# Performance work log

Hardware: AMD Instinct MI355X
Metric: run time of the kernel (lower is better)

## Reference

```python
import jax, jax.numpy as jnp
import numpy as np

EMBED_DIM = 512
NUM_HEADS = 8
HEAD_DIM = EMBED_DIM // NUM_HEADS


def setup_inputs() -> dict:
    key = jax.random.key(0)
    ks = jax.random.split(key, 6)
    B, S, D = 2, 4096, EMBED_DIM
    scale = 1.0 / np.sqrt(D)
    inputs = jax.random.normal(ks[0], (B, S, D), dtype=jnp.float32)
    Wq = jax.random.normal(ks[1], (D, D), dtype=jnp.float32) * scale
    Wk = jax.random.normal(ks[2], (D, D), dtype=jnp.float32) * scale
    Wv = jax.random.normal(ks[3], (D, D), dtype=jnp.float32) * scale
    Wo = jax.random.normal(ks[4], (D, D), dtype=jnp.float32) * scale
    zeros = jnp.zeros((D,), dtype=jnp.float32)
    return {"inputs": inputs, "Wq": Wq, "bq": zeros, "Wk": Wk, "bk": zeros,
            "Wv": Wv, "bv": zeros, "Wo": Wo, "bo": zeros}


def _split_heads(x, B, S):
    # [B,S,D] -> [B,H,S,hd]
    return x.reshape(B, S, NUM_HEADS, HEAD_DIM).transpose(0, 2, 1, 3)


def reference(inputs, Wq, bq, Wk, bk, Wv, bv, Wo, bo):
    B, S, D = inputs.shape
    q = _split_heads(inputs @ Wq + bq, B, S)
    k = _split_heads(inputs @ Wk + bk, B, S)
    v = _split_heads(inputs @ Wv + bv, B, S)
    scale = 1.0 / jnp.sqrt(jnp.asarray(HEAD_DIM, dtype=inputs.dtype))
    # full [B,H,S,S] score matrix, as in the original naive SDPA
    scores = jnp.einsum('bhqd,bhkd->bhqk', q, k) * scale
    weights = jax.nn.softmax(scores, axis=-1)
    attn = jnp.einsum('bhqk,bhkd->bhqd', weights, v)
    attn = attn.transpose(0, 2, 1, 3).reshape(B, S, D)
    return attn @ Wo + bo
```

## Files before the change

kernel.cpp:

```cpp
#include <hip/hip_runtime.h>
#include <hip/hip_bf16.h>
#include <stdint.h>


typedef __bf16 bf16x8 __attribute__((ext_vector_type(8)));
typedef float f32x4 __attribute__((ext_vector_type(4)));
typedef float f32x16 __attribute__((ext_vector_type(16)));

using as1_void = __attribute__((address_space(1))) void;
using as3_void = __attribute__((address_space(3))) void;

__device__ __forceinline__ void gload16(const void* g, void* l) {
    __builtin_amdgcn_global_load_lds((const as1_void*)g, (as3_void*)l, 16, 0, 0);
}

__device__ __forceinline__ f32x4 mfma16(bf16x8 a, bf16x8 b, f32x4 c) {
    return __builtin_amdgcn_mfma_f32_16x16x32_bf16(a, b, c, 0, 0, 0);
}

__device__ __forceinline__ f32x16 mfma32(bf16x8 a, bf16x8 b, f32x16 c) {
    return __builtin_amdgcn_mfma_f32_32x32x16_bf16(a, b, c, 0, 0, 0);
}

__device__ __forceinline__ uint32_t pkbf(float a, float b) {
    union { __hip_bfloat16 h[2]; uint32_t u; } r;
    r.h[0] = __float2bfloat16(a);
    r.h[1] = __float2bfloat16(b);
    return r.u;
}

__device__ __forceinline__ void pl32swap(uint32_t& a, uint32_t& b) {
#if __has_builtin(__builtin_amdgcn_permlane32_swap)
    typedef unsigned int uint32x2_t __attribute__((ext_vector_type(2)));
    uint32x2_t r = __builtin_amdgcn_permlane32_swap(a, b, false, false);
    a = r[0];
    b = r[1];
#else
    asm volatile("v_permlane32_swap_b32 %0, %1" : "+v"(a), "+v"(b));
#endif
}

__global__ void cvt_all(const float* __restrict__ X, __hip_bfloat16* __restrict__ Xb,
                        const float* __restrict__ w0, const float* __restrict__ w1,
                        const float* __restrict__ w2, const float* __restrict__ w3,
                        __hip_bfloat16* __restrict__ o0, __hip_bfloat16* __restrict__ o1,
                        __hip_bfloat16* __restrict__ o2, __hip_bfloat16* __restrict__ o3) {
    __shared__ float t[32][33];
    const int bid = blockIdx.x, tid = threadIdx.x;
    if (bid < 1024) {
        const float* W; __hip_bfloat16* O;
        switch (bid >> 8) {
            case 0: W = w0; O = o0; break;
            case 1: W = w1; O = o1; break;
            case 2: W = w2; O = o2; break;
            default: W = w3; O = o3; break;
        }
        int rem = bid & 255;
        int n0 = (rem & 15) * 32, k0 = (rem >> 4) * 32;
        int tx = tid & 31, ty = tid >> 5;
        for (int j = 0; j < 4; ++j)
            t[ty + 8 * j][tx] = W[(size_t)(k0 + ty + 8 * j) * 512 + n0 + tx];
        __syncthreads();
        for (int j = 0; j < 4; ++j)
            O[(size_t)(n0 + ty + 8 * j) * 512 + k0 + tx] = __float2bfloat16(t[tx][ty + 8 * j]);
    } else {
        int i = ((bid - 1024) * 256 + tid) * 4;
        float4 v = *reinterpret_cast<const float4*>(X + i);
        uint2 u;
        u.x = pkbf(v.x, v.y);
        u.y = pkbf(v.z, v.w);
        *reinterpret_cast<uint2*>(Xb + i) = u;
    }
}

__global__ __launch_bounds__(256, 2) void gemm_qkv(
    const __hip_bfloat16* __restrict__ A, const __hip_bfloat16* __restrict__ Bt,
    const float* __restrict__ bq, const float* __restrict__ bk, const float* __restrict__ bv,
    __hip_bfloat16* __restrict__ Qb, __hip_bfloat16* __restrict__ Kb,
    __hip_bfloat16* __restrict__ Vtb, float qs)
{
    const int K = 512;
    __shared__ __hip_bfloat16 Abuf[128 * 32];
    __shared__ __hip_bfloat16 Bbuf[128 * 32];
    const int tid = threadIdx.x, w = tid >> 6, lane = tid & 63;
    const int col = lane & 15, quad = lane >> 4;
    const int wr = w >> 1, wc = w & 1;
    const int tileN = blockIdx.x * 128, tileM = blockIdx.y * 128;

    f32x4 acc[4][4] = {};

    for (int k0 = 0; k0 < K; k0 += 32) {
        for (int i = 0; i < 2; ++i) {
            int g = w * 2 + i;
            int chunk = g * 64 + lane;
            int row = chunk >> 2, c8 = chunk & 3;
            gload16(A + (size_t)(tileM + row) * K + k0 + c8 * 8, Abuf + g * 512);
            gload16(Bt + (size_t)(tileN + row) * K + k0 + c8 * 8, Bbuf + g * 512);
        }
        __syncthreads();
        bf16x8 af[4], bfr[4];
        for (int mt = 0; mt < 4; ++mt)
            af[mt] = *reinterpret_cast<const bf16x8*>(Abuf + (wr * 64 + mt * 16 + col) * 32 + quad * 8);
        for (int nt = 0; nt < 4; ++nt)
            bfr[nt] = *reinterpret_cast<const bf16x8*>(Bbuf + (wc * 64 + nt * 16 + col) * 32 + quad * 8);
        for (int mt = 0; mt < 4; ++mt)
            for (int nt = 0; nt < 4; ++nt)
                acc[mt][nt] = mfma16(af[mt], bfr[nt], acc[mt][nt]);
        __syncthreads();
    }

    const int seg = (tileN + wc * 64) >> 9;
    const float* bias = (seg == 0) ? bq : (seg == 1) ? bk : bv;
    const float scale = (seg == 0) ? qs : 1.0f;
    __hip_bfloat16* outp = (seg == 0) ? Qb : (seg == 1) ? Kb : Vtb;

    for (int mt = 0; mt < 4; ++mt) {
        for (int nt = 0; nt < 4; ++nt) {
            int n = tileN + wc * 64 + nt * 16 + col;
            int nn = n & 511, h = nn >> 6, d = nn & 63;
            float bn = bias[nn];
            for (int r = 0; r < 4; ++r) {
                int m = tileM + wr * 64 + mt * 16 + quad * 4 + r;
                int b = m >> 12, s = m & 4095;
                float v = (acc[mt][nt][r] + bn) * scale;
                size_t off;
                if (seg < 2) off = (((size_t)(b * 8 + h) * 4096 + s) << 6) + d;
                else         off = (((size_t)(b * 8 + h) * 64 + d) << 12) + s;
                outp[off] = __float2bfloat16(v);
            }
        }
    }
}

__global__ __launch_bounds__(256, 2) void gemm_out(
    const __hip_bfloat16* __restrict__ A, const __hip_bfloat16* __restrict__ Bt,
    const float* __restrict__ bias, float* __restrict__ out)
{
    const int N = 512, K = 512;
    __shared__ __hip_bfloat16 Abuf[128 * 32];
    __shared__ __hip_bfloat16 Bbuf[64 * 32];
    const int tid = threadIdx.x, w = tid >> 6, lane = tid & 63;
    const int col = lane & 15, quad = lane >> 4;
    const int tileN = blockIdx.x * 64, tileM = blockIdx.y * 128;

    f32x4 acc[2][4] = {};

    for (int k0 = 0; k0 < K; k0 += 32) {
        for (int i = 0; i < 2; ++i) {
            int g = w * 2 + i;
            int chunk = g * 64 + lane;
            int row = chunk >> 2, c8 = chunk & 3;
            gload16(A + (size_t)(tileM + row) * K + k0 + c8 * 8, Abuf + g * 512);
        }
        {
            int row = tid >> 2, c8 = tid & 3;
            gload16(Bt + (size_t)(tileN + row) * K + k0 + c8 * 8, Bbuf + tid * 8);
        }
        __syncthreads();
        bf16x8 af[2], bfr[4];
        for (int mt = 0; mt < 2; ++mt)
            af[mt] = *reinterpret_cast<const bf16x8*>(Abuf + (w * 32 + mt * 16 + col) * 32 + quad * 8);
        for (int nt = 0; nt < 4; ++nt)
            bfr[nt] = *reinterpret_cast<const bf16x8*>(Bbuf + (nt * 16 + col) * 32 + quad * 8);
        for (int mt = 0; mt < 2; ++mt)
            for (int nt = 0; nt < 4; ++nt)
                acc[mt][nt] = mfma16(af[mt], bfr[nt], acc[mt][nt]);
        __syncthreads();
    }

    for (int mt = 0; mt < 2; ++mt) {
        for (int nt = 0; nt < 4; ++nt) {
            int n = tileN + nt * 16 + col;
            float bn = bias[n];
            for (int r = 0; r < 4; ++r) {
                int m = tileM + w * 32 + mt * 16 + quad * 4 + r;
                out[(size_t)m * N + n] = acc[mt][nt][r] + bn;
            }
        }
    }
}

__global__ __launch_bounds__(256, 2) void flash(
    const __hip_bfloat16* __restrict__ Q,
    const __hip_bfloat16* __restrict__ Kq,
    const __hip_bfloat16* __restrict__ Vt,
    __hip_bfloat16* __restrict__ attnb)
{
    __shared__ __hip_bfloat16 KT[2][4096];
    __shared__ __hip_bfloat16 VB[2][4096];

    const int bh = blockIdx.y, b = bh >> 3, hq = bh & 7;
    const int tid = threadIdx.x, w = tid >> 6, lane = tid & 63;
    const int l31 = lane & 31, hh = lane >> 5, l7 = lane & 7;
    const int q0 = blockIdx.x * 128 + w * 32;

    const __hip_bfloat16* Qh = Q + (size_t)bh * 4096 * 64;
    const __hip_bfloat16* Kh = Kq + (size_t)bh * 4096 * 64;
    const __hip_bfloat16* Vh = Vt + (size_t)bh * 64 * 4096;

    bf16x8 aq[4];
#pragma unroll
    for (int dk = 0; dk < 4; ++dk)
        aq[dk] = *reinterpret_cast<const bf16x8*>(
            Qh + (size_t)(q0 + l31) * 64 + dk * 16 + hh * 8);

    const __hip_bfloat16* ksrc[2];
    const __hip_bfloat16* vsrc[2];
    int ldsoff[2];
#pragma unroll
    for (int i = 0; i < 2; ++i) {
        int c = i * 256 + tid;
        int row = c >> 3, s8 = (c & 7) ^ (row & 7);
        ksrc[i] = Kh + row * 64 + s8 * 8;
        vsrc[i] = Vh + (size_t)row * 4096 + s8 * 8;
        ldsoff[i] = (i * 256 + w * 64) * 8;
    }

    bf16x8 ones;
#pragma unroll
    for (int j = 0; j < 8; ++j) ones[j] = (__bf16)1.0f;

    const f32x16 z16 = {};
    f32x16 o[2] = {};
    f32x16 lacc = {};
    f32x16 sc[2][2];

    gload16(ksrc[0], &KT[0][ldsoff[0]]);
    gload16(ksrc[1], &KT[0][ldsoff[1]]);
    gload16(vsrc[0], &VB[0][ldsoff[0]]);
    gload16(vsrc[1], &VB[0][ldsoff[1]]);
    gload16(ksrc[0] + 4096, &KT[1][ldsoff[0]]);
    gload16(ksrc[1] + 4096, &KT[1][ldsoff[1]]);
    __syncthreads();

#define QK_STEP(KR_, SP2_)                                                      \
    _Pragma("unroll")                                                           \
    for (int kg = 0; kg < 2; ++kg) {                                            \
        _Pragma("unroll")                                                       \
        for (int dk = 0; dk < 4; ++dk) {                                        \
            bf16x8 ak = *reinterpret_cast<const bf16x8*>(                       \
                &KT[KR_][(kg * 32 + l31) * 64 + (((dk * 2 + hh) ^ l7) << 3)]);  \
            sc[SP2_][kg] = (dk == 0) ? mfma32(ak, aq[0], z16)                   \
                                     : mfma32(ak, aq[dk], sc[SP2_][kg]);        \
        }                                                                       \
    }

#define SOFTMAX_EXCHANGE(SP_)                                                   \
    uint32_t U[8][2];                                                           \
    _Pragma("unroll")                                                           \
    for (int kg = 0; kg < 2; ++kg) {                                            \
        f32x16 v = sc[SP_][kg];                                                 \
        _Pragma("unroll")                                                       \
        for (int rr = 0; rr < 4; ++rr) {                                        \
            U[kg * 4 + rr][0] = pkbf(__builtin_amdgcn_exp2f(v[rr * 4 + 0]),     \
                                     __builtin_amdgcn_exp2f(v[rr * 4 + 1]));    \
            U[kg * 4 + rr][1] = pkbf(__builtin_amdgcn_exp2f(v[rr * 4 + 2]),     \
                                     __builtin_amdgcn_exp2f(v[rr * 4 + 3]));    \
        }                                                                       \
    }                                                                           \
    bf16x8 bp[4];                                                               \
    _Pragma("unroll")                                                           \
    for (int kb = 0; kb < 4; ++kb) {                                            \
        _Pragma("unroll")                                                       \
        for (int t2 = 0; t2 < 2; ++t2)                                          \
            pl32swap(U[2 * kb][t2], U[2 * kb + 1][t2]);                         \
        union { uint32_t u[4]; bf16x8 v8; } cc;                                 \
        cc.u[0] = U[2 * kb][0];     cc.u[1] = U[2 * kb][1];                     \
        cc.u[2] = U[2 * kb + 1][0]; cc.u[3] = U[2 * kb + 1][1];                 \
        bp[kb] = cc.v8;                                                         \
    }

#define PV_STEP(VR_)                                                            \
    _Pragma("unroll")                                                           \
    for (int dg = 0; dg < 2; ++dg) {                                            \
        _Pragma("unroll")                                                       \
        for (int kb = 0; kb < 4; ++kb) {                                        \
            bf16x8 av = *reinterpret_cast<const bf16x8*>(                       \
                &VB[VR_][(dg * 32 + l31) * 64 + (((kb * 2 + hh) ^ l7) << 3)]);  \
            o[dg] = mfma32(av, bp[kb], o[dg]);                                  \
        }                                                                       \
    }                                                                           \
    _Pragma("unroll")                                                           \
    for (int kb = 0; kb < 4; ++kb) lacc = mfma32(ones, bp[kb], lacc);

    QK_STEP(0, 0)
    __syncthreads();

#define FLASH_BODY(T_, P_)                                                      \
    {                                                                           \
        const int kt_ = (T_);                                                   \
        int kk = kt_ + 2; if (kk > 63) kk = 63;                                 \
        gload16(ksrc[0] + (size_t)kk * 4096, &KT[(P_)][ldsoff[0]]);             \
        gload16(ksrc[1] + (size_t)kk * 4096, &KT[(P_)][ldsoff[1]]);             \
        gload16(vsrc[0] + (size_t)(kt_ + 1) * 64, &VB[1 - (P_)][ldsoff[0]]);    \
        gload16(vsrc[1] + (size_t)(kt_ + 1) * 64, &VB[1 - (P_)][ldsoff[1]]);    \
        SOFTMAX_EXCHANGE(P_)                                                    \
        QK_STEP(1 - (P_), 1 - (P_))                                             \
        PV_STEP(P_)                                                             \
        __syncthreads();                                                        \
    }

    FLASH_BODY(0, 0)
    for (int kth = 0; kth < 31; ++kth) {
        FLASH_BODY(2 * kth + 1, 1)
        FLASH_BODY(2 * kth + 2, 0)
    }
    {
        SOFTMAX_EXCHANGE(1)
        PV_STEP(1)
    }
#undef FLASH_BODY
#undef PV_STEP
#undef SOFTMAX_EXCHANGE
#undef QK_STEP

    {
        float inv = 1.0f / lacc[0];
        int s = q0 + l31;
        __hip_bfloat16* dst = attnb + ((size_t)b * 4096 + s) * 512 + hq * 64;
#pragma unroll
        for (int dg = 0; dg < 2; ++dg)
#pragma unroll
            for (int rr = 0; rr < 4; ++rr) {
                uint2 u;
                u.x = pkbf(o[dg][rr * 4 + 0] * inv, o[dg][rr * 4 + 1] * inv);
                u.y = pkbf(o[dg][rr * 4 + 2] * inv, o[dg][rr * 4 + 3] * inv);
                *reinterpret_cast<uint2*>(dst + dg * 32 + rr * 8 + hh * 4) = u;
            }
    }
}

extern "C" void kernel_launch(void* const* d_in, const int* in_sizes, int n_in,
                              void* d_out, int out_size, void* d_ws, size_t ws_size,
                              hipStream_t stream) {
    const float* X  = (const float*)d_in[0];
    const float* Wq = (const float*)d_in[1];
    const float* bq = (const float*)d_in[2];
    const float* Wk = (const float*)d_in[3];
    const float* bk = (const float*)d_in[4];
    const float* Wv = (const float*)d_in[5];
    const float* bv = (const float*)d_in[6];
    const float* Wo = (const float*)d_in[7];
    const float* bo = (const float*)d_in[8];
    float* out = (float*)d_out;

    char* ws = (char*)d_ws;
    __hip_bfloat16* Xb  = (__hip_bfloat16*)(ws);
    __hip_bfloat16* Wqt = (__hip_bfloat16*)(ws + ((size_t)8 << 20));
    __hip_bfloat16* Wkt = Wqt + 512 * 512;
    __hip_bfloat16* Wvt = Wkt + 512 * 512;
    __hip_bfloat16* Wot = Wvt + 512 * 512;
    __hip_bfloat16* Qb  = (__hip_bfloat16*)(ws + ((size_t)10 << 20));
    __hip_bfloat16* Kb  = (__hip_bfloat16*)(ws + ((size_t)18 << 20));
    __hip_bfloat16* Vtb = (__hip_bfloat16*)(ws + ((size_t)26 << 20));
    __hip_bfloat16* Atb = (__hip_bfloat16*)(ws + ((size_t)34 << 20));

    cvt_all<<<5120, 256, 0, stream>>>(X, Xb, Wq, Wk, Wv, Wo, Wqt, Wkt, Wvt, Wot);

    const float qs = 0.125f * 1.4426950408889634f;
    gemm_qkv<<<dim3(12, 64), 256, 0, stream>>>(Xb, Wqt, bq, bk, bv, Qb, Kb, Vtb, qs);
    flash<<<dim3(32, 16), 256, 0, stream>>>(Qb, Kb, Vtb, Atb);
    gemm_out<<<dim3(8, 64), 256, 0, stream>>>(Atb, Wot, bo, out);
}
```

Measured before the change: 209.6 us.

## Split attention keys into two halves across blocks and merge partial outputs

The flash kernel grid gains a z dimension of 2, so each block processes only half of the key/value sequence. Each block writes a normalized partial output plus its row sum. A new merge kernel then combines the two partials, weighted by their row sums, before the output projection. This doubles the number of blocks to improve GPU occupancy and latency hiding, at the cost of an extra kernel launch, extra global traffic for the partial outputs, and reuse of workspace and output buffers as scratch.

```diff
diff --git a/kernel.cpp b/kernel.cpp
--- a/kernel.cpp
+++ b/kernel.cpp
@@ -184,12 +184,16 @@
     const __hip_bfloat16* __restrict__ Q,
     const __hip_bfloat16* __restrict__ Kq,
     const __hip_bfloat16* __restrict__ Vt,
-    __hip_bfloat16* __restrict__ attnb)
+    __hip_bfloat16* __restrict__ O1,
+    __hip_bfloat16* __restrict__ O2,
+    float* __restrict__ Lb)
 {
     __shared__ __hip_bfloat16 KT[2][4096];
     __shared__ __hip_bfloat16 VB[2][4096];
 
     const int bh = blockIdx.y, b = bh >> 3, hq = bh & 7;
+    const int kvh = blockIdx.z;
+    const int base = kvh * 32;
     const int tid = threadIdx.x, w = tid >> 6, lane = tid & 63;
     const int l31 = lane & 31, hh = lane >> 5, l7 = lane & 7;
     const int q0 = blockIdx.x * 128 + w * 32;
@@ -225,12 +229,12 @@
     f32x16 lacc = {};
     f32x16 sc[2][2];
 
-    gload16(ksrc[0], &KT[0][ldsoff[0]]);
-    gload16(ksrc[1], &KT[0][ldsoff[1]]);
-    gload16(vsrc[0], &VB[0][ldsoff[0]]);
-    gload16(vsrc[1], &VB[0][ldsoff[1]]);
-    gload16(ksrc[0] + 4096, &KT[1][ldsoff[0]]);
-    gload16(ksrc[1] + 4096, &KT[1][ldsoff[1]]);
+    gload16(ksrc[0] + (size_t)base * 4096, &KT[0][ldsoff[0]]);
+    gload16(ksrc[1] + (size_t)base * 4096, &KT[0][ldsoff[1]]);
+    gload16(vsrc[0] + (size_t)base * 64, &VB[0][ldsoff[0]]);
+    gload16(vsrc[1] + (size_t)base * 64, &VB[0][ldsoff[1]]);
+    gload16(ksrc[0] + (size_t)(base + 1) * 4096, &KT[1][ldsoff[0]]);
+    gload16(ksrc[1] + (size_t)(base + 1) * 4096, &KT[1][ldsoff[1]]);
     __syncthreads();
 
 #define QK_STEP(KR_, SP2_)                                                      \
@@ -289,7 +293,7 @@
 #define FLASH_BODY(T_, P_)                                                      \
     {                                                                           \
         const int kt_ = (T_);                                                   \
-        int kk = kt_ + 2; if (kk > 63) kk = 63;                                 \
+        int kk = kt_ + 2; if (kk > base + 31) kk = base + 31;                   \
         gload16(ksrc[0] + (size_t)kk * 4096, &KT[(P_)][ldsoff[0]]);             \
         gload16(ksrc[1] + (size_t)kk * 4096, &KT[(P_)][ldsoff[1]]);             \
         gload16(vsrc[0] + (size_t)(kt_ + 1) * 64, &VB[1 - (P_)][ldsoff[0]]);    \
@@ -300,10 +304,10 @@
         __syncthreads();                                                        \
     }
 
-    FLASH_BODY(0, 0)
-    for (int kth = 0; kth < 31; ++kth) {
-        FLASH_BODY(2 * kth + 1, 1)
-        FLASH_BODY(2 * kth + 2, 0)
+    FLASH_BODY(base + 0, 0)
+    for (int kth = 0; kth < 15; ++kth) {
+        FLASH_BODY(base + 2 * kth + 1, 1)
+        FLASH_BODY(base + 2 * kth + 2, 0)
     }
     {
         SOFTMAX_EXCHANGE(1)
@@ -315,9 +319,11 @@
 #undef QK_STEP
 
     {
-        float inv = 1.0f / lacc[0];
+        float l = lacc[0];
+        float inv = 1.0f / l;
         int s = q0 + l31;
-        __hip_bfloat16* dst = attnb + ((size_t)b * 4096 + s) * 512 + hq * 64;
+        __hip_bfloat16* Od = kvh ? O2 : O1;
+        __hip_bfloat16* dst = Od + ((size_t)b * 4096 + s) * 512 + hq * 64;
 #pragma unroll
         for (int dg = 0; dg < 2; ++dg)
 #pragma unroll
@@ -327,7 +333,41 @@
                 u.y = pkbf(o[dg][rr * 4 + 2] * inv, o[dg][rr * 4 + 3] * inv);
                 *reinterpret_cast<uint2*>(dst + dg * 32 + rr * 8 + hh * 4) = u;
             }
-    }
+        if (hh == 0)
+            Lb[((size_t)kvh * 16 + bh) * 4096 + s] = l;
+    }
+}
+
+__global__ __launch_bounds__(256) void merge_po(
+    const __hip_bfloat16* __restrict__ O1, const __hip_bfloat16* __restrict__ O2,
+    const float* __restrict__ Lb, __hip_bfloat16* __restrict__ Am)
+{
+    int c = blockIdx.x * 256 + threadIdx.x;
+    int flat = c * 8;
+    int d = flat & 511, s = (flat >> 9) & 4095, b = flat >> 21;
+    int bh = b * 8 + (d >> 6);
+    float l1 = Lb[(size_t)bh * 4096 + s];
+    float l2 = Lb[(size_t)(16 + bh) * 4096 + s];
+    float rs = 1.0f / (l1 + l2);
+    float w1 = l1 * rs, w2 = l2 * rs;
+    bf16x8 a = *reinterpret_cast<const bf16x8*>(O1 + flat);
+    bf16x8 bb = *reinterpret_cast<const bf16x8*>(O2 + flat);
+    uint2 u;
+    float r0 = w1 * (float)a[0] + w2 * (float)bb[0];
+    float r1 = w1 * (float)a[1] + w2 * (float)bb[1];
+    float r2 = w1 * (float)a[2] + w2 * (float)bb[2];
+    float r3 = w1 * (float)a[3] + w2 * (float)bb[3];
+    float r4 = w1 * (float)a[4] + w2 * (float)bb[4];
+    float r5 = w1 * (float)a[5] + w2 * (float)bb[5];
+    float r6 = w1 * (float)a[6] + w2 * (float)bb[6];
+    float r7 = w1 * (float)a[7] + w2 * (float)bb[7];
+    u.x = pkbf(r0, r1);
+    u.y = pkbf(r2, r3);
+    uint2 v;
+    v.x = pkbf(r4, r5);
+    v.y = pkbf(r6, r7);
+    uint4 uu = {u.x, u.y, v.x, v.y};
+    *reinterpret_cast<uint4*>(Am + flat) = uu;
 }
 
 extern "C" void kernel_launch(void* const* d_in, const int* in_sizes, int n_in,
@@ -353,12 +393,16 @@
     __hip_bfloat16* Qb  = (__hip_bfloat16*)(ws + ((size_t)10 << 20));
     __hip_bfloat16* Kb  = (__hip_bfloat16*)(ws + ((size_t)18 << 20));
     __hip_bfloat16* Vtb = (__hip_bfloat16*)(ws + ((size_t)26 << 20));
-    __hip_bfloat16* Atb = (__hip_bfloat16*)(ws + ((size_t)34 << 20));
+    __hip_bfloat16* O1  = (__hip_bfloat16*)(ws + ((size_t)34 << 20));
+    __hip_bfloat16* O2  = (__hip_bfloat16*)(ws);
+    __hip_bfloat16* Am  = (__hip_bfloat16*)(ws + ((size_t)10 << 20));
+    float* Lb = (float*)d_out;
 
     cvt_all<<<5120, 256, 0, stream>>>(X, Xb, Wq, Wk, Wv, Wo, Wqt, Wkt, Wvt, Wot);
 
     const float qs = 0.125f * 1.4426950408889634f;
     gemm_qkv<<<dim3(12, 64), 256, 0, stream>>>(Xb, Wqt, bq, bk, bv, Qb, Kb, Vtb, qs);
-    flash<<<dim3(32, 16), 256, 0, stream>>>(Qb, Kb, Vtb, Atb);
-    gemm_out<<<dim3(8, 64), 256, 0, stream>>>(Atb, Wot, bo, out);
-}
+    flash<<<dim3(32, 16, 2), 256, 0, stream>>>(Qb, Kb, Vtb, O1, O2, Lb);
+    merge_po<<<2048, 256, 0, stream>>>(O1, O2, Lb, Am);
+    gemm_out<<<dim3(8, 64), 256, 0, stream>>>(Am, Wot, bo, out);
+}
```

Result: slower. 221.2 us (+5.5%).

## Process two K/V tiles per barrier window with doubled LDS buffers

Applied to the files above, without the earlier changes.

Restructures the flash attention main loop so each synchronization window loads and processes two 64-key tiles instead of one. K and V buffers are doubled to 2x8192 elements, and the prefetch of the next window's two tiles is issued before the current window's QK, softmax and PV work. This halves the number of __syncthreads barriers and drops the staggered software pipeline in which softmax for one tile overlapped QK of the next. The cost is LDS use rising to 64KB per block, which may reduce occupancy below the two-blocks-per-CU launch bound, and the removed cross-tile overlap.

```diff
diff --git a/kernel.cpp b/kernel.cpp
--- a/kernel.cpp
+++ b/kernel.cpp
@@ -186,8 +186,8 @@
     const __hip_bfloat16* __restrict__ Vt,
     __hip_bfloat16* __restrict__ attnb)
 {
-    __shared__ __hip_bfloat16 KT[2][4096];
-    __shared__ __hip_bfloat16 VB[2][4096];
+    __shared__ __hip_bfloat16 KT[2][8192];
+    __shared__ __hip_bfloat16 VB[2][8192];
 
     const int bh = blockIdx.y, b = bh >> 3, hq = bh & 7;
     const int tid = threadIdx.x, w = tid >> 6, lane = tid & 63;
@@ -223,96 +223,105 @@
     const f32x16 z16 = {};
     f32x16 o[2] = {};
     f32x16 lacc = {};
-    f32x16 sc[2][2];
-
-    gload16(ksrc[0], &KT[0][ldsoff[0]]);
-    gload16(ksrc[1], &KT[0][ldsoff[1]]);
-    gload16(vsrc[0], &VB[0][ldsoff[0]]);
-    gload16(vsrc[1], &VB[0][ldsoff[1]]);
-    gload16(ksrc[0] + 4096, &KT[1][ldsoff[0]]);
-    gload16(ksrc[1] + 4096, &KT[1][ldsoff[1]]);
+    f32x16 sc0[2], sc1[2];
+
+#pragma unroll
+    for (int t2 = 0; t2 < 2; ++t2)
+#pragma unroll
+        for (int i = 0; i < 2; ++i) {
+            gload16(ksrc[i] + (size_t)t2 * 4096, &KT[0][t2 * 4096 + ldsoff[i]]);
+            gload16(vsrc[i] + (size_t)t2 * 64,  &VB[0][t2 * 4096 + ldsoff[i]]);
+        }
     __syncthreads();
 
-#define QK_STEP(KR_, SP2_)                                                      \
+#define QK_T(P_, T2_, SC_)                                                      \
     _Pragma("unroll")                                                           \
     for (int kg = 0; kg < 2; ++kg) {                                            \
         _Pragma("unroll")                                                       \
         for (int dk = 0; dk < 4; ++dk) {                                        \
             bf16x8 ak = *reinterpret_cast<const bf16x8*>(                       \
-                &KT[KR_][(kg * 32 + l31) * 64 + (((dk * 2 + hh) ^ l7) << 3)]);  \
-            sc[SP2_][kg] = (dk == 0) ? mfma32(ak, aq[0], z16)                   \
-                                     : mfma32(ak, aq[dk], sc[SP2_][kg]);        \
-        }                                                                       \
-    }
-
-#define SOFTMAX_EXCHANGE(SP_)                                                   \
-    uint32_t U[8][2];                                                           \
-    _Pragma("unroll")                                                           \
-    for (int kg = 0; kg < 2; ++kg) {                                            \
-        f32x16 v = sc[SP_][kg];                                                 \
+                &KT[P_][(T2_) * 4096 + (kg * 32 + l31) * 64 +                   \
+                        (((dk * 2 + hh) ^ l7) << 3)]);                          \
+            SC_[kg] = (dk == 0) ? mfma32(ak, aq[0], z16)                        \
+                                : mfma32(ak, aq[dk], SC_[kg]);                  \
+        }                                                                       \
+    }
+
+#define SM_T(SC_, BP_)                                                          \
+    {                                                                           \
+        uint32_t U[8][2];                                                       \
         _Pragma("unroll")                                                       \
-        for (int rr = 0; rr < 4; ++rr) {                                        \
-            U[kg * 4 + rr][0] = pkbf(__builtin_amdgcn_exp2f(v[rr * 4 + 0]),     \
-                                     __builtin_amdgcn_exp2f(v[rr * 4 + 1]));    \
-            U[kg * 4 + rr][1] = pkbf(__builtin_amdgcn_exp2f(v[rr * 4 + 2]),     \
-                                     __builtin_amdgcn_exp2f(v[rr * 4 + 3]));    \
-        }                                                                       \
-    }                                                                           \
-    bf16x8 bp[4];                                                               \
-    _Pragma("unroll")                                                           \
-    for (int kb = 0; kb < 4; ++kb) {                                            \
+        for (int kg = 0; kg < 2; ++kg) {                                        \
+            f32x16 v = SC_[kg];                                                 \
+            _Pragma("unroll")                                                   \
+            for (int rr = 0; rr < 4; ++rr) {                                    \
+                U[kg * 4 + rr][0] = pkbf(__builtin_amdgcn_exp2f(v[rr * 4 + 0]), \
+                                         __builtin_amdgcn_exp2f(v[rr * 4 + 1]));\
+                U[kg * 4 + rr][1] = pkbf(__builtin_amdgcn_exp2f(v[rr * 4 + 2]), \
+                                         __builtin_amdgcn_exp2f(v[rr * 4 + 3]));\
+            }                                                                   \
+        }                                                                       \
         _Pragma("unroll")                                                       \
-        for (int t2 = 0; t2 < 2; ++t2)                                          \
-            pl32swap(U[2 * kb][t2], U[2 * kb + 1][t2]);                         \
-        union { uint32_t u[4]; bf16x8 v8; } cc;                                 \
-        cc.u[0] = U[2 * kb][0];     cc.u[1] = U[2 * kb][1];                     \
-        cc.u[2] = U[2 * kb + 1][0]; cc.u[3] = U[2 * kb + 1][1];                 \
-        bp[kb] = cc.v8;                                                         \
-    }
-
-#define PV_STEP(VR_)                                                            \
+        for (int kb = 0; kb < 4; ++kb) {                                        \
+            pl32swap(U[2 * kb][0], U[2 * kb + 1][0]);                           \
+            pl32swap(U[2 * kb][1], U[2 * kb + 1][1]);                           \
+            union { uint32_t u[4]; bf16x8 v8; } cc;                             \
+            cc.u[0] = U[2 * kb][0];     cc.u[1] = U[2 * kb][1];                 \
+            cc.u[2] = U[2 * kb + 1][0]; cc.u[3] = U[2 * kb + 1][1];             \
+            BP_[kb] = cc.v8;                                                    \
+        }                                                                       \
+    }
+
+#define PV_T(P_, T2_, BP_)                                                      \
     _Pragma("unroll")                                                           \
     for (int dg = 0; dg < 2; ++dg) {                                            \
         _Pragma("unroll")                                                       \
         for (int kb = 0; kb < 4; ++kb) {                                        \
             bf16x8 av = *reinterpret_cast<const bf16x8*>(                       \
-                &VB[VR_][(dg * 32 + l31) * 64 + (((kb * 2 + hh) ^ l7) << 3)]);  \
-            o[dg] = mfma32(av, bp[kb], o[dg]);                                  \
+                &VB[P_][(T2_) * 4096 + (dg * 32 + l31) * 64 +                   \
+                        (((kb * 2 + hh) ^ l7) << 3)]);                          \
+            o[dg] = mfma32(av, BP_[kb], o[dg]);                                 \
         }                                                                       \
     }                                                                           \
     _Pragma("unroll")                                                           \
-    for (int kb = 0; kb < 4; ++kb) lacc = mfma32(ones, bp[kb], lacc);
-
-    QK_STEP(0, 0)
-    __syncthreads();
-
-#define FLASH_BODY(T_, P_)                                                      \
+    for (int kb = 0; kb < 4; ++kb) lacc = mfma32(ones, BP_[kb], lacc);
+
+#define WINDOW(W_, P_)                                                          \
     {                                                                           \
-        const int kt_ = (T_);                                                   \
-        int kk = kt_ + 2; if (kk > 63) kk = 63;                                 \
-        gload16(ksrc[0] + (size_t)kk * 4096, &KT[(P_)][ldsoff[0]]);             \
-        gload16(ksrc[1] + (size_t)kk * 4096, &KT[(P_)][ldsoff[1]]);             \
-        gload16(vsrc[0] + (size_t)(kt_ + 1) * 64, &VB[1 - (P_)][ldsoff[0]]);    \
-        gload16(vsrc[1] + (size_t)(kt_ + 1) * 64, &VB[1 - (P_)][ldsoff[1]]);    \
-        SOFTMAX_EXCHANGE(P_)                                                    \
-        QK_STEP(1 - (P_), 1 - (P_))                                             \
-        PV_STEP(P_)                                                             \
+        const int t0_ = 2 * (W_);                                               \
+        int ka = t0_ + 2; if (ka > 62) ka = 62;                                 \
+        int kb2 = t0_ + 3; if (kb2 > 63) kb2 = 63;                              \
+        gload16(ksrc[0] + (size_t)ka * 4096, &KT[1 - (P_)][ldsoff[0]]);         \
+        gload16(ksrc[1] + (size_t)ka * 4096, &KT[1 - (P_)][ldsoff[1]]);         \
+        gload16(ksrc[0] + (size_t)kb2 * 4096, &KT[1 - (P_)][4096 + ldsoff[0]]); \
+        gload16(ksrc[1] + (size_t)kb2 * 4096, &KT[1 - (P_)][4096 + ldsoff[1]]); \
+        gload16(vsrc[0] + (size_t)ka * 64, &VB[1 - (P_)][ldsoff[0]]);           \
+        gload16(vsrc[1] + (size_t)ka * 64, &VB[1 - (P_)][ldsoff[1]]);           \
+        gload16(vsrc[0] + (size_t)kb2 * 64, &VB[1 - (P_)][4096 + ldsoff[0]]);   \
+        gload16(vsrc[1] + (size_t)kb2 * 64, &VB[1 - (P_)][4096 + ldsoff[1]]);   \
+        QK_T(P_, 0, sc0)                                                        \
+        QK_T(P_, 1, sc1)                                                        \
+        {                                                                       \
+            bf16x8 bpA[4];                                                      \
+            SM_T(sc0, bpA)                                                      \
+            PV_T(P_, 0, bpA)                                                    \
+        }                                                                       \
+        {                                                                       \
+            bf16x8 bpB[4];                                                      \
+            SM_T(sc1, bpB)                                                      \
+            PV_T(P_, 1, bpB)                                                    \
+        }                                                                       \
         __syncthreads();                                                        \
     }
 
-    FLASH_BODY(0, 0)
-    for (int kth = 0; kth < 31; ++kth) {
-        FLASH_BODY(2 * kth + 1, 1)
-        FLASH_BODY(2 * kth + 2, 0)
-    }
-    {
-        SOFTMAX_EXCHANGE(1)
-        PV_STEP(1)
-    }
-#undef FLASH_BODY
-#undef PV_STEP
-#undef SOFTMAX_EXCHANGE
-#undef QK_STEP
+    for (int wh = 0; wh < 16; ++wh) {
+        WINDOW(2 * wh, 0)
+        WINDOW(2 * wh + 1, 1)
+    }
+#undef WINDOW
+#undef PV_T
+#undef SM_T
+#undef QK_T
 
     {
         float inv = 1.0f / lacc[0];
```

Result: slower. 215.9 us (+3.0%).

## Load K/V fragments directly from global into registers, dropping LDS staging

Applied to the files above, without the earlier changes.

Replaces the shared-memory double-buffered K/V tiles and block barriers with per-wave direct global loads of MFMA operand fragments, prefetching the next K tile into a register double buffer. This removes the barrier sync and LDS traffic. In exchange, each wave redundantly fetches the same K/V data, which raises global/L2 traffic and register pressure, and the V loads are issued just before use.

```diff
diff --git a/kernel.cpp b/kernel.cpp
--- a/kernel.cpp
+++ b/kernel.cpp
@@ -186,12 +186,9 @@
     const __hip_bfloat16* __restrict__ Vt,
     __hip_bfloat16* __restrict__ attnb)
 {
-    __shared__ __hip_bfloat16 KT[2][4096];
-    __shared__ __hip_bfloat16 VB[2][4096];
-
     const int bh = blockIdx.y, b = bh >> 3, hq = bh & 7;
     const int tid = threadIdx.x, w = tid >> 6, lane = tid & 63;
-    const int l31 = lane & 31, hh = lane >> 5, l7 = lane & 7;
+    const int l31 = lane & 31, hh = lane >> 5;
     const int q0 = blockIdx.x * 128 + w * 32;
 
     const __hip_bfloat16* Qh = Q + (size_t)bh * 4096 * 64;
@@ -204,17 +201,8 @@
         aq[dk] = *reinterpret_cast<const bf16x8*>(
             Qh + (size_t)(q0 + l31) * 64 + dk * 16 + hh * 8);
 
-    const __hip_bfloat16* ksrc[2];
-    const __hip_bfloat16* vsrc[2];
-    int ldsoff[2];
-#pragma unroll
-    for (int i = 0; i < 2; ++i) {
-        int c = i * 256 + tid;
-        int row = c >> 3, s8 = (c & 7) ^ (row & 7);
-        ksrc[i] = Kh + row * 64 + s8 * 8;
-        vsrc[i] = Vh + (size_t)row * 4096 + s8 * 8;
-        ldsoff[i] = (i * 256 + w * 64) * 8;
-    }
+    const __hip_bfloat16* kb0 = Kh + (size_t)l31 * 64 + hh * 8;
+    const __hip_bfloat16* vb0 = Vh + (size_t)l31 * 4096 + hh * 8;
 
     bf16x8 ones;
 #pragma unroll
@@ -223,96 +211,77 @@
     const f32x16 z16 = {};
     f32x16 o[2] = {};
     f32x16 lacc = {};
-    f32x16 sc[2][2];
-
-    gload16(ksrc[0], &KT[0][ldsoff[0]]);
-    gload16(ksrc[1], &KT[0][ldsoff[1]]);
-    gload16(vsrc[0], &VB[0][ldsoff[0]]);
-    gload16(vsrc[1], &VB[0][ldsoff[1]]);
-    gload16(ksrc[0] + 4096, &KT[1][ldsoff[0]]);
-    gload16(ksrc[1] + 4096, &KT[1][ldsoff[1]]);
-    __syncthreads();
-
-#define QK_STEP(KR_, SP2_)                                                      \
-    _Pragma("unroll")                                                           \
-    for (int kg = 0; kg < 2; ++kg) {                                            \
-        _Pragma("unroll")                                                       \
-        for (int dk = 0; dk < 4; ++dk) {                                        \
-            bf16x8 ak = *reinterpret_cast<const bf16x8*>(                       \
-                &KT[KR_][(kg * 32 + l31) * 64 + (((dk * 2 + hh) ^ l7) << 3)]);  \
-            sc[SP2_][kg] = (dk == 0) ? mfma32(ak, aq[0], z16)                   \
-                                     : mfma32(ak, aq[dk], sc[SP2_][kg]);        \
-        }                                                                       \
-    }
-
-#define SOFTMAX_EXCHANGE(SP_)                                                   \
-    uint32_t U[8][2];                                                           \
-    _Pragma("unroll")                                                           \
-    for (int kg = 0; kg < 2; ++kg) {                                            \
-        f32x16 v = sc[SP_][kg];                                                 \
-        _Pragma("unroll")                                                       \
-        for (int rr = 0; rr < 4; ++rr) {                                        \
-            U[kg * 4 + rr][0] = pkbf(__builtin_amdgcn_exp2f(v[rr * 4 + 0]),     \
-                                     __builtin_amdgcn_exp2f(v[rr * 4 + 1]));    \
-            U[kg * 4 + rr][1] = pkbf(__builtin_amdgcn_exp2f(v[rr * 4 + 2]),     \
-                                     __builtin_amdgcn_exp2f(v[rr * 4 + 3]));    \
-        }                                                                       \
-    }                                                                           \
-    bf16x8 bp[4];                                                               \
-    _Pragma("unroll")                                                           \
-    for (int kb = 0; kb < 4; ++kb) {                                            \
-        _Pragma("unroll")                                                       \
-        for (int t2 = 0; t2 < 2; ++t2)                                          \
-            pl32swap(U[2 * kb][t2], U[2 * kb + 1][t2]);                         \
-        union { uint32_t u[4]; bf16x8 v8; } cc;                                 \
-        cc.u[0] = U[2 * kb][0];     cc.u[1] = U[2 * kb][1];                     \
-        cc.u[2] = U[2 * kb + 1][0]; cc.u[3] = U[2 * kb + 1][1];                 \
-        bp[kb] = cc.v8;                                                         \
-    }
-
-#define PV_STEP(VR_)                                                            \
-    _Pragma("unroll")                                                           \
-    for (int dg = 0; dg < 2; ++dg) {                                            \
-        _Pragma("unroll")                                                       \
-        for (int kb = 0; kb < 4; ++kb) {                                        \
-            bf16x8 av = *reinterpret_cast<const bf16x8*>(                       \
-                &VB[VR_][(dg * 32 + l31) * 64 + (((kb * 2 + hh) ^ l7) << 3)]);  \
-            o[dg] = mfma32(av, bp[kb], o[dg]);                                  \
-        }                                                                       \
-    }                                                                           \
-    _Pragma("unroll")                                                           \
-    for (int kb = 0; kb < 4; ++kb) lacc = mfma32(ones, bp[kb], lacc);
-
-    QK_STEP(0, 0)
-    __syncthreads();
-
-#define FLASH_BODY(T_, P_)                                                      \
-    {                                                                           \
-        const int kt_ = (T_);                                                   \
-        int kk = kt_ + 2; if (kk > 63) kk = 63;                                 \
-        gload16(ksrc[0] + (size_t)kk * 4096, &KT[(P_)][ldsoff[0]]);             \
-        gload16(ksrc[1] + (size_t)kk * 4096, &KT[(P_)][ldsoff[1]]);             \
-        gload16(vsrc[0] + (size_t)(kt_ + 1) * 64, &VB[1 - (P_)][ldsoff[0]]);    \
-        gload16(vsrc[1] + (size_t)(kt_ + 1) * 64, &VB[1 - (P_)][ldsoff[1]]);    \
-        SOFTMAX_EXCHANGE(P_)                                                    \
-        QK_STEP(1 - (P_), 1 - (P_))                                             \
-        PV_STEP(P_)                                                             \
-        __syncthreads();                                                        \
-    }
-
-    FLASH_BODY(0, 0)
-    for (int kth = 0; kth < 31; ++kth) {
-        FLASH_BODY(2 * kth + 1, 1)
-        FLASH_BODY(2 * kth + 2, 0)
-    }
-    {
-        SOFTMAX_EXCHANGE(1)
-        PV_STEP(1)
+
+    bf16x8 ak0[2][4], ak1[2][4];
+
+#pragma unroll
+    for (int kg = 0; kg < 2; ++kg)
+#pragma unroll
+        for (int dk = 0; dk < 4; ++dk)
+            ak0[kg][dk] = *reinterpret_cast<const bf16x8*>(
+                kb0 + kg * (32 * 64) + dk * 16);
+
+#define FLASH_BODY(T_, AKC_, AKN_)                                             \
+    {                                                                          \
+        const int t_ = (T_);                                                   \
+        const int tn_ = (t_ < 63) ? t_ + 1 : 63;                               \
+        bf16x8 av[2][4];                                                       \
+        _Pragma("unroll")                                                      \
+        for (int dg = 0; dg < 2; ++dg)                                         \
+            _Pragma("unroll")                                                  \
+            for (int kb = 0; kb < 4; ++kb)                                     \
+                av[dg][kb] = *reinterpret_cast<const bf16x8*>(                 \
+                    vb0 + (size_t)dg * (32 * 4096) + t_ * 64 + kb * 16);       \
+        _Pragma("unroll")                                                      \
+        for (int kg = 0; kg < 2; ++kg)                                         \
+            _Pragma("unroll")                                                  \
+            for (int dk = 0; dk < 4; ++dk)                                     \
+                AKN_[kg][dk] = *reinterpret_cast<const bf16x8*>(               \
+                    kb0 + (size_t)tn_ * 4096 + kg * (32 * 64) + dk * 16);      \
+        f32x16 sc[2];                                                          \
+        _Pragma("unroll")                                                      \
+        for (int kg = 0; kg < 2; ++kg) {                                       \
+            _Pragma("unroll")                                                  \
+            for (int dk = 0; dk < 4; ++dk)                                     \
+                sc[kg] = (dk == 0) ? mfma32(AKC_[kg][0], aq[0], z16)           \
+                                   : mfma32(AKC_[kg][dk], aq[dk], sc[kg]);     \
+        }                                                                      \
+        uint32_t U[8][2];                                                      \
+        _Pragma("unroll")                                                      \
+        for (int kg = 0; kg < 2; ++kg) {                                       \
+            f32x16 v = sc[kg];                                                 \
+            _Pragma("unroll")                                                  \
+            for (int rr = 0; rr < 4; ++rr) {                                   \
+                U[kg * 4 + rr][0] = pkbf(__builtin_amdgcn_exp2f(v[rr * 4 + 0]),\
+                                         __builtin_amdgcn_exp2f(v[rr * 4 + 1]));\
+                U[kg * 4 + rr][1] = pkbf(__builtin_amdgcn_exp2f(v[rr * 4 + 2]),\
+                                         __builtin_amdgcn_exp2f(v[rr * 4 + 3]));\
+            }                                                                  \
+        }                                                                      \
+        bf16x8 bp[4];                                                          \
+        _Pragma("unroll")                                                      \
+        for (int kb = 0; kb < 4; ++kb) {                                       \
+            pl32swap(U[2 * kb][0], U[2 * kb + 1][0]);                          \
+            pl32swap(U[2 * kb][1], U[2 * kb + 1][1]);                          \
+            union { uint32_t u[4]; bf16x8 v8; } cc;                            \
+            cc.u[0] = U[2 * kb][0];     cc.u[1] = U[2 * kb][1];                \
+            cc.u[2] = U[2 * kb + 1][0]; cc.u[3] = U[2 * kb + 1][1];            \
+            bp[kb] = cc.v8;                                                    \
+        }                                                                      \
+        _Pragma("unroll")                                                      \
+        for (int dg = 0; dg < 2; ++dg)                                         \
+            _Pragma("unroll")                                                  \
+            for (int kb = 0; kb < 4; ++kb)                                     \
+                o[dg] = mfma32(av[dg][kb], bp[kb], o[dg]);                     \
+        _Pragma("unroll")                                                      \
+        for (int kb = 0; kb < 4; ++kb) lacc = mfma32(ones, bp[kb], lacc);      \
+    }
+
+    for (int t2 = 0; t2 < 32; ++t2) {
+        FLASH_BODY(2 * t2, ak0, ak1)
+        FLASH_BODY(2 * t2 + 1, ak1, ak0)
     }
 #undef FLASH_BODY
-#undef PV_STEP
-#undef SOFTMAX_EXCHANGE
-#undef QK_STEP
 
     {
         float inv = 1.0f / lacc[0];
```

Result: slower. 354.3 us (+69.0%).
